# Optimization experiments

Measured on AMD Instinct MI355X. Metric: run time of the kernel, lower is better.

Reference implementation:

```python
import jax, jax.numpy as jnp
import numpy as np

B, NPG, EG, F, EDIM, ESM = 32, 256, 2048, 128, 16, 1280
NN, E = B * NPG, B * EG
H, Dh = 4, 128
HD = H * Dh


def setup_inputs() -> dict:
    key = jax.random.key(0)
    ks = jax.random.split(key, 32)
    x = jax.random.normal(ks[0], (NN, F), jnp.float32)
    edge_attr = jax.random.normal(ks[1], (E, EDIM), jnp.float32)
    off = jnp.repeat(jnp.arange(B, dtype=jnp.int32) * NPG, EG)
    src = off + jax.random.randint(ks[2], (E,), 0, NPG, dtype=jnp.int32)
    dst = off + jax.random.randint(ks[3], (E,), 0, NPG, dtype=jnp.int32)
    edge_index = jnp.stack([src, dst])
    batch_index = jnp.repeat(jnp.arange(B, dtype=jnp.int32), NPG)
    esm = jax.random.normal(ks[4], (B, ESM), jnp.float32)
    g = lambda i, shp: jax.random.normal(ks[i], shp, jnp.float32) * 0.05
    return dict(
        x=x, edge_attr=edge_attr, edge_index=edge_index, batch_index=batch_index,
        esm2_embeddings=esm,
        Wq=g(5, (5, F, HD)), bq=g(6, (5, HD)), Wk=g(7, (5, F, HD)), bk=g(8, (5, HD)),
        Wv=g(9, (5, F, HD)), bv=g(10, (5, HD)), We=g(11, (5, EDIM, HD)),
        Wskip=g(12, (5, F, HD)), bskip=g(13, (5, HD)), Wbeta=g(14, (5, 3 * HD)),
        Wt=g(15, (5, HD, F)), bt=g(16, (5, F)),
        gamma=1.0 + g(17, (5, F)), beta_bn=g(18, (5, F)), rmean=g(19, (5, F)),
        rvar=0.5 + jax.random.uniform(ks[20], (5, F)),
        pw=g(21, (2, F)),
        W1=g(22, (2 * F + ESM, 512)), b1=g(23, (512,)),
        W2=g(24, (512, 256)), b2=g(25, (256,)),
        W3=g(26, (256, 10)), b3=g(27, (10,)))


def _forward(x, edge_attr, esm, Wq, bq, Wk, bk, Wv, bv, We, Wskip, bskip, Wbeta,
             Wt, bt, gamma, beta_bn, rmean, rvar, pw, W1, b1, W2, b2, W3, b3,
             src, dst, batch_index):
    scale = 1.0 / jnp.sqrt(jnp.float32(Dh))

    def conv(h, li, emask):
        # PyG TransformerConv(beta=True, edge_dim) + Linear + ReLU + BatchNorm(eval)
        q = (h @ Wq[li] + bq[li]).reshape(NN, H, Dh)
        k = (h @ Wk[li] + bk[li]).reshape(NN, H, Dh)
        v = (h @ Wv[li] + bv[li]).reshape(NN, H, Dh)
        e = (edge_attr @ We[li]).reshape(E, H, Dh)   # lin_edge, bias=False
        kj = k[src] + e                               # [E,H,Dh]
        a = jnp.einsum('ehd,ehd->eh', q[dst], kj) * scale
        a = jnp.where(emask[:, None], a, -1e30)
        m = jnp.maximum(jax.ops.segment_max(a, dst, num_segments=NN), -1e30)
        ea = jnp.exp(a - m[dst]) * emask[:, None]
        den = jax.ops.segment_sum(ea, dst, num_segments=NN)
        attn = ea / jnp.maximum(den[dst], 1e-16)      # scatter-softmax over dst
        msg = (v[src] + e) * attn[..., None]
        out = jax.ops.segment_sum(msg, dst, num_segments=NN).reshape(NN, HD)
        xr = h @ Wskip[li] + bskip[li]                # root/skip path
        bta = jax.nn.sigmoid(jnp.concatenate([out, xr, out - xr], -1) @ Wbeta[li])[:, None]
        h2 = bta * xr + (1.0 - bta) * out
        h2 = jax.nn.relu(h2 @ Wt[li] + bt[li])
        return (h2 - rmean[li]) / jnp.sqrt(rvar[li] + 1e-5) * gamma[li] + beta_bn[li]

    nmask = jnp.ones((NN,), bool)
    emask = jnp.ones((E,), bool)
    h = conv(x, 0, emask)
    k_list = [NPG // 2, NPG // 4]  # ratio=0.5 applied twice
    reps = []
    for i in range(4):
        h = conv(h, i + 1, emask)
        if i % 2 == 0:  # top_k_every_n = 2
            p = i // 2
            w = pw[p]
            s = jnp.tanh((h @ w) / jnp.linalg.norm(w))      # TopKPooling score
            s_m = jnp.where(nmask, s, -jnp.inf)
            ranks = jnp.argsort(jnp.argsort(-s_m.reshape(B, NPG), axis=1), axis=1).reshape(-1)
            keep = (ranks < k_list[p]) & nmask
            h = h * s[:, None] * keep[:, None]
            nmask = keep
            emask = emask & keep[src] & keep[dst]
            cnt = jax.ops.segment_sum(keep.astype(h.dtype), batch_index, num_segments=B)
            gmax = jax.ops.segment_max(jnp.where(keep[:, None], h, -1e30), batch_index, num_segments=B)
            gmean = jax.ops.segment_sum(h * keep[:, None], batch_index, num_segments=B) / jnp.maximum(cnt, 1.0)[:, None]
            reps.append(jnp.concatenate([gmax, gmean], 1))
    g = reps[0] + reps[1]
    g = jnp.concatenate([g, esm], 1)
    g = jax.nn.relu(g @ W1 + b1)   # dropout(p=0.8) is identity at inference
    g = jax.nn.relu(g @ W2 + b2)
    return g @ W3 + b3


def reference(x, edge_attr, edge_index, batch_index, esm2_embeddings,
              Wq, bq, Wk, bk, Wv, bv, We, Wskip, bskip, Wbeta, Wt, bt,
              gamma, beta_bn, rmean, rvar, pw, W1, b1, W2, b2, W3, b3):
    src, dst = edge_index[0], edge_index[1]
    return _forward(x, edge_attr, esm2_embeddings, Wq, bq, Wk, bk, Wv, bv, We,
                    Wskip, bskip, Wbeta, Wt, bt, gamma, beta_bn, rmean, rvar,
                    pw, W1, b1, W2, b2, W3, b3, src, dst, batch_index)
```

## Files before the change

kernel.cpp:

```cpp
#include <hip/hip_runtime.h>
#include <math.h>

#define BB 32
#define NPGC 256
#define FF 128
#define EDIMC 16
#define ESMC 1280
#define NNODE 8192
#define NEDGE 65536
#define EGC 2048
#define NH 4
#define DH 128
#define HDIM 512

typedef __attribute__((ext_vector_type(8))) short bf16x8;
typedef __attribute__((ext_vector_type(4))) float f32x4;

__device__ __forceinline__ float waveReduceSum(float v) {
#pragma unroll
    for (int o = 32; o > 0; o >>= 1) v += __shfl_down(v, o);
    return v;
}

__device__ __forceinline__ unsigned short f2b(float f) {
    unsigned u = __builtin_bit_cast(unsigned, f);
    return (unsigned short)((u + 0x7fffu + ((u >> 16) & 1u)) >> 16);
}
__device__ __forceinline__ unsigned pack2(float lo, float hi) {
    return (unsigned)f2b(lo) | ((unsigned)f2b(hi) << 16);
}
__device__ __forceinline__ float2 b2f2(unsigned u) {
    float lo = __builtin_bit_cast(float, u << 16);
    float hi = __builtin_bit_cast(float, u & 0xffff0000u);
    return make_float2(lo, hi);
}

__global__ __launch_bounds__(256) void k_convert_setup(
    const float* __restrict__ x, const float* __restrict__ Wq,
    const float* __restrict__ Wk, const float* __restrict__ Wv,
    const float* __restrict__ Wsk, const float* __restrict__ Wt,
    const float* __restrict__ W1, const float* __restrict__ W2,
    unsigned short* __restrict__ xb, unsigned short* __restrict__ wqb,
    unsigned short* __restrict__ wkb, unsigned short* __restrict__ wvb,
    unsigned short* __restrict__ wskb, unsigned short* __restrict__ wtb,
    unsigned short* __restrict__ w1b, unsigned short* __restrict__ w2b,
    const int* __restrict__ dst, int* __restrict__ emask, int* __restrict__ nmask,
    int* __restrict__ coff, int* __restrict__ ceid) {
    __shared__ int cntS[NPGC];
    __shared__ int scanS[NPGC];
    __shared__ int offS[NPGC];
    if (blockIdx.x >= 12800) {
        int g = blockIdx.x - 12800, t = threadIdx.x;
        cntS[t] = 0;
        nmask[g * NPGC + t] = 1;
        __syncthreads();
        int base = g * EGC;
#pragma unroll
        for (int i = 0; i < EGC / 256; ++i) {
            int e = base + i * 256 + t;
            emask[e] = 1;
            atomicAdd(&cntS[dst[e] - g * NPGC], 1);
        }
        __syncthreads();
        scanS[t] = cntS[t];
        __syncthreads();
        for (int off = 1; off < NPGC; off <<= 1) {
            int v = scanS[t];
            if (t >= off) v += scanS[t - off];
            __syncthreads();
            scanS[t] = v;
            __syncthreads();
        }
        int excl = scanS[t] - cntS[t];
        offS[t] = excl;
        coff[g * NPGC + t] = base + excl;
        if (g == 0 && t == 0) coff[NNODE] = NEDGE;
        cntS[t] = 0;
        __syncthreads();
#pragma unroll
        for (int i = 0; i < EGC / 256; ++i) {
            int e = base + i * 256 + t;
            int d = dst[e] - g * NPGC;
            int pos = atomicAdd(&cntS[d], 1);
            ceid[base + offS[d] + pos] = e;
        }
        return;
    }
    int idx = blockIdx.x * 256 + threadIdx.x;
    if (idx < 1048576) { xb[idx] = f2b(x[idx]); return; }
    idx -= 1048576;
    if (idx < 1048576) {
        int fam = idx >> 18, local = idx & 262143;
        int li = local >> 16, rem = local & 65535;
        int n = rem >> 7, k = rem & 127;
        const float* S = (fam == 0) ? Wq : (fam == 1) ? Wk : (fam == 2) ? Wv : Wsk;
        unsigned short* D = (fam == 0) ? wqb : (fam == 1) ? wkb : (fam == 2) ? wvb : wskb;
        D[local] = f2b(S[(size_t)li * 65536 + (size_t)k * 512 + n]);
        return;
    }
    idx -= 1048576;
    if (idx < 262144) {
        int li = idx >> 16, rem = idx & 65535;
        int n = rem >> 9, k = rem & 511;
        wtb[idx] = f2b(Wt[(size_t)li * 65536 + (size_t)k * 128 + n]);
        return;
    }
    idx -= 262144;
    if (idx < 786432) {
        int n = idx / 1536, k = idx % 1536;
        w1b[idx] = f2b(W1[(size_t)k * 512 + n]);
        return;
    }
    idx -= 786432;
    {
        int n = idx >> 9, k = idx & 511;
        w2b[idx] = f2b(W2[(size_t)k * 256 + n]);
    }
}

__global__ __launch_bounds__(256) void k_qkvs_mfma(
    const unsigned short* __restrict__ hb,
    const unsigned short* __restrict__ wq, const unsigned short* __restrict__ wk,
    const unsigned short* __restrict__ wv, const unsigned short* __restrict__ wsk,
    const float* __restrict__ bq, const float* __restrict__ bk,
    const float* __restrict__ bv, const float* __restrict__ bsk,
    unsigned short* __restrict__ oq, unsigned short* __restrict__ ok,
    unsigned short* __restrict__ ov, unsigned short* __restrict__ osk) {
    const unsigned short* W;
    const float* bias;
    unsigned short* out;
    if (blockIdx.z == 0) { W = wq; bias = bq; out = oq; }
    else if (blockIdx.z == 1) { W = wk; bias = bk; out = ok; }
    else if (blockIdx.z == 2) { W = wv; bias = bv; out = ov; }
    else { W = wsk; bias = bsk; out = osk; }
    int lane = threadIdx.x & 63, wave = threadIdx.x >> 6;
    int quad = lane >> 4, m = lane & 15;
    int xcdx = blockIdx.x;
    int g = (xcdx & 7) + 8 * ((xcdx >> 3) & 3);
    int half = xcdx >> 5;
    int rowbase = g * NPGC + half * 128 + (wave >> 1) * 64;
    int colbase = blockIdx.y * 128 + (wave & 1) * 64;
    f32x4 zero = {0.f, 0.f, 0.f, 0.f};
    f32x4 acc[4][4];
#pragma unroll
    for (int i = 0; i < 4; ++i)
#pragma unroll
        for (int j = 0; j < 4; ++j) acc[i][j] = zero;
#pragma unroll
    for (int ks = 0; ks < 4; ++ks) {
        int k0 = ks * 32 + quad * 8;
        bf16x8 af[4], bfr[4];
#pragma unroll
        for (int tm = 0; tm < 4; ++tm)
            af[tm] = *(const bf16x8*)(hb + (size_t)(rowbase + tm * 16 + m) * FF + k0);
#pragma unroll
        for (int tn = 0; tn < 4; ++tn)
            bfr[tn] = *(const bf16x8*)(W + (size_t)(colbase + tn * 16 + m) * FF + k0);
#pragma unroll
        for (int tm = 0; tm < 4; ++tm)
#pragma unroll
            for (int tn = 0; tn < 4; ++tn)
                acc[tm][tn] = __builtin_amdgcn_mfma_f32_16x16x32_bf16(af[tm], bfr[tn],
                                                                      acc[tm][tn], 0, 0, 0);
    }
#pragma unroll
    for (int tn = 0; tn < 4; ++tn) {
        int col = colbase + tn * 16 + m;
        float bc = bias[col];
#pragma unroll
        for (int tm = 0; tm < 4; ++tm)
#pragma unroll
            for (int r = 0; r < 4; ++r)
                out[(size_t)(rowbase + tm * 16 + quad * 4 + r) * HDIM + col] =
                    f2b(acc[tm][tn][r] + bc);
    }
}

__global__ __launch_bounds__(128) void k_out_mfma(
    const unsigned short* __restrict__ h2b, const unsigned short* __restrict__ wt,
    const float* __restrict__ bt_, const float* __restrict__ gam_,
    const float* __restrict__ bet_, const float* __restrict__ rme_,
    const float* __restrict__ rva_, float* __restrict__ hout,
    unsigned short* __restrict__ hbf) {
    int lane = threadIdx.x & 63, wave = threadIdx.x >> 6;
    int quad = lane >> 4, m = lane & 15;
    int bi = blockIdx.x;
    int g = (bi & 7) + 8 * ((bi >> 3) & 3);
    int sub = bi >> 5;
    int rowbase = g * NPGC + sub * 32;
    int colbase = wave * 64;
    f32x4 zero = {0.f, 0.f, 0.f, 0.f};
    f32x4 acc[2][4];
#pragma unroll
    for (int i = 0; i < 2; ++i)
#pragma unroll
        for (int j = 0; j < 4; ++j) acc[i][j] = zero;
    for (int ks = 0; ks < 16; ++ks) {
        int k0 = ks * 32 + quad * 8;
        bf16x8 af[2], bfr[4];
#pragma unroll
        for (int tm = 0; tm < 2; ++tm)
            af[tm] = *(const bf16x8*)(h2b + (size_t)(rowbase + tm * 16 + m) * HDIM + k0);
#pragma unroll
        for (int tn = 0; tn < 4; ++tn)
            bfr[tn] = *(const bf16x8*)(wt + (size_t)(colbase + tn * 16 + m) * HDIM + k0);
#pragma unroll
        for (int tm = 0; tm < 2; ++tm)
#pragma unroll
            for (int tn = 0; tn < 4; ++tn)
                acc[tm][tn] = __builtin_amdgcn_mfma_f32_16x16x32_bf16(af[tm], bfr[tn],
                                                                      acc[tm][tn], 0, 0, 0);
    }
#pragma unroll
    for (int tn = 0; tn < 4; ++tn) {
        int col = colbase + tn * 16 + m;
        float bc = bt_[col];
        float sc = gam_[col] * rsqrtf(rva_[col] + 1e-5f);
        float sh = bet_[col] - rme_[col] * sc;
#pragma unroll
        for (int tm = 0; tm < 2; ++tm)
#pragma unroll
            for (int r = 0; r < 4; ++r) {
                size_t o = (size_t)(rowbase + tm * 16 + quad * 4 + r) * FF + col;
                float v = fmaxf(acc[tm][tn][r] + bc, 0.f) * sc + sh;
                hout[o] = v;
                hbf[o] = f2b(v);
            }
    }
}

__global__ __launch_bounds__(256) void k_mlp_mfma(const unsigned short* __restrict__ A,
                                                  const unsigned short* __restrict__ Wt,
                                                  float* __restrict__ cp,
                                                  int N, int K, int KS) {
    int lane = threadIdx.x & 63, wave = threadIdx.x >> 6;
    int quad = lane >> 4, m = lane & 15;
    int colbase = blockIdx.x * 256 + wave * 64;
    int kc = K / KS;
    int k0b = blockIdx.y * kc;
    f32x4 zero = {0.f, 0.f, 0.f, 0.f};
    f32x4 acc[2][4];
#pragma unroll
    for (int i = 0; i < 2; ++i)
#pragma unroll
        for (int j = 0; j < 4; ++j) acc[i][j] = zero;
    for (int ks = 0; ks < kc / 32; ++ks) {
        int k0 = k0b + ks * 32 + quad * 8;
        bf16x8 a0 = *(const bf16x8*)(A + (size_t)m * K + k0);
        bf16x8 a1 = *(const bf16x8*)(A + (size_t)(16 + m) * K + k0);
        bf16x8 bfr[4];
#pragma unroll
        for (int tn = 0; tn < 4; ++tn)
            bfr[tn] = *(const bf16x8*)(Wt + (size_t)(colbase + tn * 16 + m) * K + k0);
#pragma unroll
        for (int tn = 0; tn < 4; ++tn) {
            acc[0][tn] = __builtin_amdgcn_mfma_f32_16x16x32_bf16(a0, bfr[tn], acc[0][tn], 0, 0, 0);
            acc[1][tn] = __builtin_amdgcn_mfma_f32_16x16x32_bf16(a1, bfr[tn], acc[1][tn], 0, 0, 0);
        }
    }
#pragma unroll
    for (int tm = 0; tm < 2; ++tm)
#pragma unroll
        for (int tn = 0; tn < 4; ++tn)
#pragma unroll
            for (int r = 0; r < 4; ++r)
                cp[((size_t)blockIdx.y * 32 + tm * 16 + quad * 4 + r) * N +
                   colbase + tn * 16 + m] = acc[tm][tn][r];
}

__global__ void k_mlp_fix(const float* __restrict__ cp, const float* __restrict__ b,
                          float* __restrict__ C, unsigned short* __restrict__ Cb,
                          int MN, int N, int KS, int relu) {
    int i = blockIdx.x * 256 + threadIdx.x;
    if (i >= MN) return;
    float acc = b[i % N];
    for (int s = 0; s < KS; ++s) acc += cp[(size_t)s * MN + i];
    if (relu) acc = fmaxf(acc, 0.f);
    C[i] = acc;
    if (Cb) Cb[i] = f2b(acc);
}

__global__ void k_g1(const float* __restrict__ pmax0, const float* __restrict__ psum0,
                     const float* __restrict__ pmax1, const float* __restrict__ psum1,
                     const float* __restrict__ esm, unsigned short* __restrict__ g1b) {
    int i = blockIdx.x * 256 + threadIdx.x;
    int r = i / 1536, c = i % 1536;
    float v;
    if (c < 128) {
        float m0 = -1e30f, m1 = -1e30f;
#pragma unroll
        for (int q = 0; q < 4; ++q) {
            m0 = fmaxf(m0, pmax0[((size_t)r * 4 + q) * 128 + c]);
            m1 = fmaxf(m1, pmax1[((size_t)r * 4 + q) * 128 + c]);
        }
        v = m0 + m1;
    } else if (c < 256) {
        int d = c - 128;
        float s0 = 0.f, s1 = 0.f;
#pragma unroll
        for (int q = 0; q < 4; ++q) {
            s0 += psum0[((size_t)r * 4 + q) * 128 + d];
            s1 += psum1[((size_t)r * 4 + q) * 128 + d];
        }
        v = s0 * (1.f / 128.f) + s1 * (1.f / 64.f);
    } else {
        v = esm[(size_t)r * ESMC + c - 256];
    }
    g1b[i] = f2b(v);
}

__global__ __launch_bounds__(256) void k_attn_wave(
    const unsigned short* __restrict__ q, const unsigned short* __restrict__ kmat,
    const unsigned short* __restrict__ vmat, const unsigned short* __restrict__ xr,
    const float* __restrict__ eattr, const float* __restrict__ We,
    const float* __restrict__ Wb,
    const int* __restrict__ src, const int* __restrict__ coff,
    const int* __restrict__ ceid, const int* __restrict__ emask,
    unsigned short* __restrict__ h2) {
    int wv = threadIdx.x >> 6, ln = threadIdx.x & 63;
    int bi = blockIdx.x;
    int g = (bi & 7) + 8 * ((bi >> 3) & 3);
    int sub = bi >> 5;
    int n = g * NPGC + sub * 4 + wv;
    int h = ln >> 4, j = ln & 15;
    int d0i = ln * 8;
    int o0 = coff[n];
    int deg = coff[n + 1] - o0;
    if (deg > 64) deg = 64;

    uint4 qu = *(const uint4*)(q + (size_t)n * HDIM + d0i);
    float2 q0 = b2f2(qu.x), q1 = b2f2(qu.y), q2 = b2f2(qu.z), q3 = b2f2(qu.w);
    float qf[8] = {q0.x, q0.y, q1.x, q1.y, q2.x, q2.y, q3.x, q3.y};

    float qp[16];
#pragma unroll
    for (int jj = 0; jj < EDIMC; ++jj) {
        const float4* wp = (const float4*)(We + (size_t)jj * HDIM + d0i);
        float4 wa = wp[0], wb4 = wp[1];
        qp[jj] = qf[0] * wa.x + qf[1] * wa.y + qf[2] * wa.z + qf[3] * wa.w +
                 qf[4] * wb4.x + qf[5] * wb4.y + qf[6] * wb4.z + qf[7] * wb4.w;
    }
#pragma unroll
    for (int off = 1; off < 16; off <<= 1)
#pragma unroll
        for (int jj = 0; jj < EDIMC; ++jj) qp[jj] += __shfl_xor(qp[jj], off);
    float qWl = qp[j];

    int e_reg = 0, s_reg = -1;
    if (ln < deg) {
        e_reg = ceid[o0 + ln];
        s_reg = emask[e_reg] ? src[e_reg] : -1;
    }

    float sc0 = -1e30f, sc1 = -1e30f, sc2 = -1e30f, sc3 = -1e30f;
    for (int i = 0; i < deg; ++i) {
        int si = __shfl(s_reg, i);
        float pr = -1e30f;
        if (si >= 0) {
            int ei = __shfl(e_reg, i);
            uint4 ku = *(const uint4*)(kmat + (size_t)si * HDIM + d0i);
            float2 k0 = b2f2(ku.x), k1 = b2f2(ku.y), k2 = b2f2(ku.z), k3 = b2f2(ku.w);
            float p = qf[0] * k0.x + qf[1] * k0.y + qf[2] * k1.x + qf[3] * k1.y +
                      qf[4] * k2.x + qf[5] * k2.y + qf[6] * k3.x + qf[7] * k3.y;
            p = fmaf(qWl, eattr[(size_t)ei * EDIMC + j], p);
            p += __shfl_xor(p, 8);
            p += __shfl_xor(p, 4);
            p += __shfl_xor(p, 2);
            p += __shfl_xor(p, 1);
            pr = p * 0.088388347648318447f;
        }
        float t0 = __shfl(pr, 0), t1 = __shfl(pr, 16);
        float t2 = __shfl(pr, 32), t3 = __shfl(pr, 48);
        if (ln == i) { sc0 = t0; sc1 = t1; sc2 = t2; sc3 = t3; }
    }

    bool valid = (ln < deg) && (s_reg >= 0);
    if (!valid) { sc0 = sc1 = sc2 = sc3 = -1e30f; }
    float m0 = sc0, m1 = sc1, m2 = sc2, m3 = sc3;
#pragma unroll
    for (int o = 32; o > 0; o >>= 1) {
        m0 = fmaxf(m0, __shfl_xor(m0, o));
        m1 = fmaxf(m1, __shfl_xor(m1, o));
        m2 = fmaxf(m2, __shfl_xor(m2, o));
        m3 = fmaxf(m3, __shfl_xor(m3, o));
    }
    float a0 = valid ? expf(sc0 - m0) : 0.f;
    float a1 = valid ? expf(sc1 - m1) : 0.f;
    float a2 = valid ? expf(sc2 - m2) : 0.f;
    float a3 = valid ? expf(sc3 - m3) : 0.f;
    float de0 = a0, de1 = a1, de2 = a2, de3 = a3;
#pragma unroll
    for (int o = 32; o > 0; o >>= 1) {
        de0 += __shfl_xor(de0, o);
        de1 += __shfl_xor(de1, o);
        de2 += __shfl_xor(de2, o);
        de3 += __shfl_xor(de3, o);
    }
    a0 /= fmaxf(de0, 1e-16f);
    a1 /= fmaxf(de1, 1e-16f);
    a2 /= fmaxf(de2, 1e-16f);
    a3 /= fmaxf(de3, 1e-16f);

    float z = 0.f;
    float out[8] = {0.f, 0.f, 0.f, 0.f, 0.f, 0.f, 0.f, 0.f};
    for (int i = 0; i < deg; ++i) {
        int si = __shfl(s_reg, i);
        if (si < 0) continue;
        float t0 = __shfl(a0, i), t1 = __shfl(a1, i);
        float t2 = __shfl(a2, i), t3 = __shfl(a3, i);
        float at = (h == 0) ? t0 : (h == 1) ? t1 : (h == 2) ? t2 : t3;
        int ei = __shfl(e_reg, i);
        z = fmaf(at, eattr[(size_t)ei * EDIMC + j], z);
        uint4 vu = *(const uint4*)(vmat + (size_t)si * HDIM + d0i);
        float2 v0 = b2f2(vu.x), v1 = b2f2(vu.y), v2 = b2f2(vu.z), v3 = b2f2(vu.w);
        out[0] = fmaf(at, v0.x, out[0]);
        out[1] = fmaf(at, v0.y, out[1]);
        out[2] = fmaf(at, v1.x, out[2]);
        out[3] = fmaf(at, v1.y, out[3]);
        out[4] = fmaf(at, v2.x, out[4]);
        out[5] = fmaf(at, v2.y, out[5]);
        out[6] = fmaf(at, v3.x, out[6]);
        out[7] = fmaf(at, v3.y, out[7]);
    }

#pragma unroll
    for (int jj = 0; jj < EDIMC; ++jj) {
        float zjj = __shfl(z, h * 16 + jj);
        const float4* wp = (const float4*)(We + (size_t)jj * HDIM + d0i);
        float4 wa = wp[0], wb4 = wp[1];
        out[0] = fmaf(zjj, wa.x, out[0]);
        out[1] = fmaf(zjj, wa.y, out[1]);
        out[2] = fmaf(zjj, wa.z, out[2]);
        out[3] = fmaf(zjj, wa.w, out[3]);
        out[4] = fmaf(zjj, wb4.x, out[4]);
        out[5] = fmaf(zjj, wb4.y, out[5]);
        out[6] = fmaf(zjj, wb4.z, out[6]);
        out[7] = fmaf(zjj, wb4.w, out[7]);
    }

    uint4 xu = *(const uint4*)(xr + (size_t)n * HDIM + d0i);
    float2 x0 = b2f2(xu.x), x1 = b2f2(xu.y), x2 = b2f2(xu.z), x3 = b2f2(xu.w);
    float xf[8] = {x0.x, x0.y, x1.x, x1.y, x2.x, x2.y, x3.x, x3.y};
    const float4* w0p = (const float4*)(Wb + d0i);
    const float4* w1p = (const float4*)(Wb + HDIM + d0i);
    const float4* w2p = (const float4*)(Wb + 2 * HDIM + d0i);
    float4 wa0 = w0p[0], wa1 = w0p[1];
    float4 wb0 = w1p[0], wb1 = w1p[1];
    float4 wc0 = w2p[0], wc1 = w2p[1];
    float w0f[8] = {wa0.x, wa0.y, wa0.z, wa0.w, wa1.x, wa1.y, wa1.z, wa1.w};
    float w1f[8] = {wb0.x, wb0.y, wb0.z, wb0.w, wb1.x, wb1.y, wb1.z, wb1.w};
    float w2f[8] = {wc0.x, wc0.y, wc0.z, wc0.w, wc1.x, wc1.y, wc1.z, wc1.w};
    float part = 0.f;
#pragma unroll
    for (int d = 0; d < 8; ++d)
        part += out[d] * w0f[d] + xf[d] * w1f[d] + (out[d] - xf[d]) * w2f[d];
#pragma unroll
    for (int o = 32; o > 0; o >>= 1) part += __shfl_xor(part, o);
    float bg = 1.f / (1.f + expf(-part));
    uint4 res;
    res.x = pack2(bg * xf[0] + (1.f - bg) * out[0], bg * xf[1] + (1.f - bg) * out[1]);
    res.y = pack2(bg * xf[2] + (1.f - bg) * out[2], bg * xf[3] + (1.f - bg) * out[3]);
    res.z = pack2(bg * xf[4] + (1.f - bg) * out[4], bg * xf[5] + (1.f - bg) * out[5]);
    res.w = pack2(bg * xf[6] + (1.f - bg) * out[6], bg * xf[7] + (1.f - bg) * out[7]);
    *(uint4*)(h2 + (size_t)n * HDIM + d0i) = res;
}

__global__ __launch_bounds__(256) void k_pool_rank(const float* __restrict__ pwv,
                                                   const float* __restrict__ h,
                                                   int* __restrict__ nmask,
                                                   int* __restrict__ emask,
                                                   const int* __restrict__ src,
                                                   const int* __restrict__ dst,
                                                   float* __restrict__ fbuf, int kc) {
    __shared__ float smS[NPGC];
    __shared__ int keepS[NPGC];
    int g = blockIdx.x, t = threadIdx.x;
    int n = g * NPGC + t;
    const float* hr = h + (size_t)n * FF;
    float nw2 = 0.f, dv = 0.f;
#pragma unroll
    for (int i = 0; i < FF; i += 4) {
        float4 wv = *(const float4*)(pwv + i);
        float4 hv = *(const float4*)(hr + i);
        nw2 += wv.x * wv.x + wv.y * wv.y + wv.z * wv.z + wv.w * wv.w;
        dv += hv.x * wv.x + hv.y * wv.y + hv.z * wv.z + hv.w * wv.w;
    }
    float s = tanhf(dv / sqrtf(nw2));
    int old = nmask[n];
    smS[t] = old ? s : -INFINITY;
    __syncthreads();
    float mys = smS[t];
    int rank = 0;
    for (int j = 0; j < NPGC; ++j) {
        float o = smS[j];
        rank += (o > mys) || (o == mys && j < t);
    }
    int kp = (rank < kc) && old;
    keepS[t] = kp;
    nmask[n] = kp;
    fbuf[n] = s * (float)kp;
    __syncthreads();
    if (emask) {
        int base = g * EGC;
        for (int ee = t; ee < EGC; ee += 256) {
            int e = base + ee;
            emask[e] = emask[e] && keepS[src[e] - g * NPGC] && keepS[dst[e] - g * NPGC];
        }
    }
}

__global__ __launch_bounds__(256) void k_pool_apply(const float* __restrict__ h,
                                                    unsigned short* __restrict__ hbf,
                                                    const float* __restrict__ fbuf,
                                                    const int* __restrict__ nmask,
                                                    float* __restrict__ pmax,
                                                    float* __restrict__ psum, int emit) {
    __shared__ float mS[4][128];
    __shared__ float sS[4][128];
    int g = blockIdx.x, seg = blockIdx.y, t = threadIdx.x;
    int l = t & 63, quar = t >> 6;
    int d2 = l * 2;
    int nbase = g * NPGC + seg * 64 + quar * 16;
    float mx0 = -1e30f, mx1 = -1e30f, sm0 = 0.f, sm1 = 0.f;
#pragma unroll 4
    for (int i = 0; i < 16; ++i) {
        int n = nbase + i;
        float f = fbuf[n];
        int kp = nmask[n];
        float2 hv = *(const float2*)(h + (size_t)n * FF + d2);
        float v0 = hv.x * f, v1 = hv.y * f;
        if (emit) *(unsigned*)(hbf + (size_t)n * FF + d2) = pack2(v0, v1);
        if (kp) {
            mx0 = fmaxf(mx0, v0);
            mx1 = fmaxf(mx1, v1);
            sm0 += v0;
            sm1 += v1;
        }
    }
    mS[quar][d2] = mx0;
    mS[quar][d2 + 1] = mx1;
    sS[quar][d2] = sm0;
    sS[quar][d2 + 1] = sm1;
    __syncthreads();
    if (t < 128) {
        float m = fmaxf(fmaxf(mS[0][t], mS[1][t]), fmaxf(mS[2][t], mS[3][t]));
        float s = sS[0][t] + sS[1][t] + sS[2][t] + sS[3][t];
        pmax[((size_t)g * 4 + seg) * 128 + t] = m;
        psum[((size_t)g * 4 + seg) * 128 + t] = s;
    }
}

__global__ __launch_bounds__(256) void k_mlp_wave(const float* __restrict__ A,
                                                  const float* __restrict__ W,
                                                  const float* __restrict__ b,
                                                  float* __restrict__ C,
                                                  int M, int N, int K, int relu) {
    int wid = (blockIdx.x * 256 + threadIdx.x) >> 6;
    int lane = threadIdx.x & 63;
    if (wid >= M * N) return;
    int r = wid / N, c = wid % N;
    const float* Arow = A + (size_t)r * K;
    float acc = 0.f;
    for (int kk = lane; kk < K; kk += 64)
        acc = fmaf(Arow[kk], W[(size_t)kk * N + c], acc);
    acc = waveReduceSum(acc);
    if (lane == 0) {
        acc += b[c];
        C[wid] = relu ? fmaxf(acc, 0.f) : acc;
    }
}

extern "C" void kernel_launch(void* const* d_in, const int* in_sizes, int n_in,
                              void* d_out, int out_size, void* d_ws, size_t ws_size,
                              hipStream_t stream) {
    const float* x = (const float*)d_in[0];
    const float* eattr = (const float*)d_in[1];
    const int* eidx = (const int*)d_in[2];
    const float* esm = (const float*)d_in[4];
    const float* Wq = (const float*)d_in[5];
    const float* bq = (const float*)d_in[6];
    const float* Wk = (const float*)d_in[7];
    const float* bk = (const float*)d_in[8];
    const float* Wv = (const float*)d_in[9];
    const float* bv = (const float*)d_in[10];
    const float* We = (const float*)d_in[11];
    const float* Wsk = (const float*)d_in[12];
    const float* bsk = (const float*)d_in[13];
    const float* Wbe = (const float*)d_in[14];
    const float* Wt = (const float*)d_in[15];
    const float* bt = (const float*)d_in[16];
    const float* gam = (const float*)d_in[17];
    const float* bet = (const float*)d_in[18];
    const float* rme = (const float*)d_in[19];
    const float* rva = (const float*)d_in[20];
    const float* pw = (const float*)d_in[21];
    const float* W1 = (const float*)d_in[22];
    const float* b1 = (const float*)d_in[23];
    const float* W2 = (const float*)d_in[24];
    const float* b2 = (const float*)d_in[25];
    const float* W3 = (const float*)d_in[26];
    const float* b3 = (const float*)d_in[27];
    const int* srcp = eidx;
    const int* dstp = eidx + NEDGE;

    char* p = (char*)d_ws;
    auto alloc = [&](size_t bytes) -> void* {
        void* r = (void*)p;
        p += (bytes + 255) & ~(size_t)255;
        return r;
    };
    float* hA = (float*)alloc((size_t)NNODE * FF * 4);
    float* hB = (float*)alloc((size_t)NNODE * FF * 4);
    float* fbuf = (float*)alloc((size_t)NNODE * 4);
    float* pmax0 = (float*)alloc((size_t)BB * 4 * 128 * 4);
    float* psum0 = (float*)alloc((size_t)BB * 4 * 128 * 4);
    float* pmax1 = (float*)alloc((size_t)BB * 4 * 128 * 4);
    float* psum1 = (float*)alloc((size_t)BB * 4 * 128 * 4);
    float* g2 = (float*)alloc((size_t)BB * 512 * 4);
    float* g3 = (float*)alloc((size_t)BB * 256 * 4);
    float* cp = (float*)alloc((size_t)8 * 32 * 512 * 4);
    int* nmask = (int*)alloc((size_t)NNODE * 4);
    int* emask = (int*)alloc((size_t)NEDGE * 4);
    int* coff = (int*)alloc((size_t)(NNODE + 1) * 4);
    int* ceid = (int*)alloc((size_t)NEDGE * 4);
    unsigned short* xb = (unsigned short*)alloc((size_t)NNODE * FF * 2);
    unsigned short* hbf = (unsigned short*)alloc((size_t)NNODE * FF * 2);
    unsigned short* qb16 = (unsigned short*)alloc((size_t)NNODE * HDIM * 2);
    unsigned short* kb16 = (unsigned short*)alloc((size_t)NNODE * HDIM * 2);
    unsigned short* vb16 = (unsigned short*)alloc((size_t)NNODE * HDIM * 2);
    unsigned short* xrb16 = (unsigned short*)alloc((size_t)NNODE * HDIM * 2);
    unsigned short* h2b16 = (unsigned short*)alloc((size_t)NNODE * HDIM * 2);
    unsigned short* wqb = (unsigned short*)alloc((size_t)4 * 65536 * 2);
    unsigned short* wkb = (unsigned short*)alloc((size_t)4 * 65536 * 2);
    unsigned short* wvb = (unsigned short*)alloc((size_t)4 * 65536 * 2);
    unsigned short* wskb = (unsigned short*)alloc((size_t)4 * 65536 * 2);
    unsigned short* wtb = (unsigned short*)alloc((size_t)4 * 65536 * 2);
    unsigned short* w1b = (unsigned short*)alloc((size_t)786432 * 2);
    unsigned short* w2b = (unsigned short*)alloc((size_t)131072 * 2);
    unsigned short* g1b = (unsigned short*)alloc((size_t)BB * 1536 * 2);
    unsigned short* g2b = (unsigned short*)alloc((size_t)BB * 512 * 2);

    k_convert_setup<<<12832, 256, 0, stream>>>(x, Wq, Wk, Wv, Wsk, Wt, W1, W2,
                                               xb, wqb, wkb, wvb, wskb, wtb, w1b, w2b,
                                               dstp, emask, nmask, coff, ceid);

    auto conv = [&](int li, const unsigned short* hin_b, float* hout) {
        dim3 gq(64, 4, 4);
        k_qkvs_mfma<<<gq, 256, 0, stream>>>(
            hin_b, wqb + (size_t)li * 65536, wkb + (size_t)li * 65536,
            wvb + (size_t)li * 65536, wskb + (size_t)li * 65536,
            bq + li * HDIM, bk + li * HDIM, bv + li * HDIM, bsk + li * HDIM,
            qb16, kb16, vb16, xrb16);
        const float* WeL = We + (size_t)li * EDIMC * HDIM;
        k_attn_wave<<<NNODE / 4, 256, 0, stream>>>(qb16, kb16, vb16, xrb16, eattr, WeL,
                                                   Wbe + (size_t)li * 3 * HDIM,
                                                   srcp, coff, ceid, emask, h2b16);
        k_out_mfma<<<NNODE / 32, 128, 0, stream>>>(
            h2b16, wtb + (size_t)li * 65536, bt + li * FF, gam + li * FF,
            bet + li * FF, rme + li * FF, rva + li * FF, hout, hbf);
    };

    auto pool = [&](int pi, const float* h, float* pmax, float* psum, int kc, bool updE,
                    int emit) {
        k_pool_rank<<<BB, 256, 0, stream>>>(pw + pi * FF, h, nmask,
                                            updE ? emask : nullptr, srcp, dstp, fbuf, kc);
        k_pool_apply<<<dim3(BB, 4), 256, 0, stream>>>(h, hbf, fbuf, nmask, pmax, psum, emit);
    };

    conv(0, xb, hA);
    conv(1, hbf, hB);
    pool(0, hB, pmax0, psum0, NPGC / 2, true, 1);
    conv(2, hbf, hA);
    conv(3, hbf, hB);
    pool(1, hB, pmax1, psum1, NPGC / 4, false, 0);

    k_g1<<<BB * 1536 / 256, 256, 0, stream>>>(pmax0, psum0, pmax1, psum1, esm, g1b);
    k_mlp_mfma<<<dim3(2, 8), 256, 0, stream>>>(g1b, w1b, cp, 512, 1536, 8);
    k_mlp_fix<<<BB * 512 / 256, 256, 0, stream>>>(cp, b1, g2, g2b, BB * 512, 512, 8, 1);
    k_mlp_mfma<<<dim3(1, 8), 256, 0, stream>>>(g2b, w2b, cp, 256, 512, 8);
    k_mlp_fix<<<BB * 256 / 256, 256, 0, stream>>>(cp, b2, g3, nullptr, BB * 256, 256, 8, 1);
    k_mlp_wave<<<(BB * 10 * 64 + 255) / 256, 256, 0, stream>>>(g3, W3, b3, (float*)d_out,
                                                               BB, 10, 256, 0);
}
```

Baseline: 505.9 us.

## Fuse attention score and aggregation into single online-softmax pass

Replaces the two-pass per-node attention (score loop, wave-wide max/sum reductions, then a separate weighted-V loop) with one loop using an online softmax. Each edge's K and V rows are loaded together, and the running max, denominator and accumulators are rescaled per edge. This removes the second traversal over edges, the per-edge broadcast shuffles and the cross-lane softmax reductions. The cost is two exponentials per edge plus a rescale of 10 accumulators. Fast __expf also replaces expf, including in the gate sigmoid.

Result: faster. 470.9 us (-6.9%).

```diff
diff --git a/kernel.cpp b/kernel.cpp
--- a/kernel.cpp
+++ b/kernel.cpp
@@ -352,76 +352,44 @@
         s_reg = emask[e_reg] ? src[e_reg] : -1;
     }
 
-    float sc0 = -1e30f, sc1 = -1e30f, sc2 = -1e30f, sc3 = -1e30f;
-    for (int i = 0; i < deg; ++i) {
-        int si = __shfl(s_reg, i);
-        float pr = -1e30f;
-        if (si >= 0) {
-            int ei = __shfl(e_reg, i);
-            uint4 ku = *(const uint4*)(kmat + (size_t)si * HDIM + d0i);
-            float2 k0 = b2f2(ku.x), k1 = b2f2(ku.y), k2 = b2f2(ku.z), k3 = b2f2(ku.w);
-            float p = qf[0] * k0.x + qf[1] * k0.y + qf[2] * k1.x + qf[3] * k1.y +
-                      qf[4] * k2.x + qf[5] * k2.y + qf[6] * k3.x + qf[7] * k3.y;
-            p = fmaf(qWl, eattr[(size_t)ei * EDIMC + j], p);
-            p += __shfl_xor(p, 8);
-            p += __shfl_xor(p, 4);
-            p += __shfl_xor(p, 2);
-            p += __shfl_xor(p, 1);
-            pr = p * 0.088388347648318447f;
-        }
-        float t0 = __shfl(pr, 0), t1 = __shfl(pr, 16);
-        float t2 = __shfl(pr, 32), t3 = __shfl(pr, 48);
-        if (ln == i) { sc0 = t0; sc1 = t1; sc2 = t2; sc3 = t3; }
-    }
-
-    bool valid = (ln < deg) && (s_reg >= 0);
-    if (!valid) { sc0 = sc1 = sc2 = sc3 = -1e30f; }
-    float m0 = sc0, m1 = sc1, m2 = sc2, m3 = sc3;
-#pragma unroll
-    for (int o = 32; o > 0; o >>= 1) {
-        m0 = fmaxf(m0, __shfl_xor(m0, o));
-        m1 = fmaxf(m1, __shfl_xor(m1, o));
-        m2 = fmaxf(m2, __shfl_xor(m2, o));
-        m3 = fmaxf(m3, __shfl_xor(m3, o));
-    }
-    float a0 = valid ? expf(sc0 - m0) : 0.f;
-    float a1 = valid ? expf(sc1 - m1) : 0.f;
-    float a2 = valid ? expf(sc2 - m2) : 0.f;
-    float a3 = valid ? expf(sc3 - m3) : 0.f;
-    float de0 = a0, de1 = a1, de2 = a2, de3 = a3;
-#pragma unroll
-    for (int o = 32; o > 0; o >>= 1) {
-        de0 += __shfl_xor(de0, o);
-        de1 += __shfl_xor(de1, o);
-        de2 += __shfl_xor(de2, o);
-        de3 += __shfl_xor(de3, o);
-    }
-    a0 /= fmaxf(de0, 1e-16f);
-    a1 /= fmaxf(de1, 1e-16f);
-    a2 /= fmaxf(de2, 1e-16f);
-    a3 /= fmaxf(de3, 1e-16f);
-
-    float z = 0.f;
+    float m = -1e30f, den = 0.f, z = 0.f;
     float out[8] = {0.f, 0.f, 0.f, 0.f, 0.f, 0.f, 0.f, 0.f};
     for (int i = 0; i < deg; ++i) {
         int si = __shfl(s_reg, i);
         if (si < 0) continue;
-        float t0 = __shfl(a0, i), t1 = __shfl(a1, i);
-        float t2 = __shfl(a2, i), t3 = __shfl(a3, i);
-        float at = (h == 0) ? t0 : (h == 1) ? t1 : (h == 2) ? t2 : t3;
         int ei = __shfl(e_reg, i);
-        z = fmaf(at, eattr[(size_t)ei * EDIMC + j], z);
+        uint4 ku = *(const uint4*)(kmat + (size_t)si * HDIM + d0i);
         uint4 vu = *(const uint4*)(vmat + (size_t)si * HDIM + d0i);
+        float eav = eattr[(size_t)ei * EDIMC + j];
+        float2 k0 = b2f2(ku.x), k1 = b2f2(ku.y), k2 = b2f2(ku.z), k3 = b2f2(ku.w);
+        float p = qf[0] * k0.x + qf[1] * k0.y + qf[2] * k1.x + qf[3] * k1.y +
+                  qf[4] * k2.x + qf[5] * k2.y + qf[6] * k3.x + qf[7] * k3.y;
+        p = fmaf(qWl, eav, p);
+        p += __shfl_xor(p, 8);
+        p += __shfl_xor(p, 4);
+        p += __shfl_xor(p, 2);
+        p += __shfl_xor(p, 1);
+        float s = p * 0.088388347648318447f;
+        float m_new = fmaxf(m, s);
+        float c = __expf(m - m_new);
+        float al = __expf(s - m_new);
+        den = den * c + al;
+        z = z * c + al * eav;
         float2 v0 = b2f2(vu.x), v1 = b2f2(vu.y), v2 = b2f2(vu.z), v3 = b2f2(vu.w);
-        out[0] = fmaf(at, v0.x, out[0]);
-        out[1] = fmaf(at, v0.y, out[1]);
-        out[2] = fmaf(at, v1.x, out[2]);
-        out[3] = fmaf(at, v1.y, out[3]);
-        out[4] = fmaf(at, v2.x, out[4]);
-        out[5] = fmaf(at, v2.y, out[5]);
-        out[6] = fmaf(at, v3.x, out[6]);
-        out[7] = fmaf(at, v3.y, out[7]);
-    }
+        out[0] = out[0] * c + al * v0.x;
+        out[1] = out[1] * c + al * v0.y;
+        out[2] = out[2] * c + al * v1.x;
+        out[3] = out[3] * c + al * v1.y;
+        out[4] = out[4] * c + al * v2.x;
+        out[5] = out[5] * c + al * v2.y;
+        out[6] = out[6] * c + al * v3.x;
+        out[7] = out[7] * c + al * v3.y;
+        m = m_new;
+    }
+    float inv = 1.f / fmaxf(den, 1e-16f);
+    z *= inv;
+#pragma unroll
+    for (int d = 0; d < 8; ++d) out[d] *= inv;
 
 #pragma unroll
     for (int jj = 0; jj < EDIMC; ++jj) {
@@ -456,7 +424,7 @@
         part += out[d] * w0f[d] + xf[d] * w1f[d] + (out[d] - xf[d]) * w2f[d];
 #pragma unroll
     for (int o = 32; o > 0; o >>= 1) part += __shfl_xor(part, o);
-    float bg = 1.f / (1.f + expf(-part));
+    float bg = 1.f / (1.f + __expf(-part));
     uint4 res;
     res.x = pack2(bg * xf[0] + (1.f - bg) * out[0], bg * xf[1] + (1.f - bg) * out[1]);
     res.y = pack2(bg * xf[2] + (1.f - bg) * out[2], bg * xf[3] + (1.f - bg) * out[3]);
```
